# Kernel optimization log

Hardware: AMD Instinct MI355X
Metric: run time of the kernel (lower is better)

Reference implementation:

```python
import jax, jax.numpy as jnp
import numpy as np

# dims: T time steps, B batch, CIN/COUT conv channels, HxW spatial, K kernel
T, B, CIN, COUT, H, Wd, K = 10, 32, 3, 64, 64, 64, 3
DECAY = 0.2      # LIF leak factor
INH = 1.625      # lateral inhibition strength (mode='threshold')


def setup_inputs() -> dict:
    key = jax.random.key(0)
    k1, k2 = jax.random.split(key)
    x = (jax.random.uniform(k1, (T, B, CIN, H, Wd)) < 0.2).astype(jnp.float32)
    W = jax.random.normal(k2, (COUT, CIN, K, K), dtype=jnp.float32)
    # normweight(): zero-mean, unit-std (biased) per output filter
    W = W - W.mean(axis=(1, 2, 3), keepdims=True)
    W = W / W.reshape(COUT, -1).std(axis=1).reshape(COUT, 1, 1, 1)
    return {"x": x, "W": W}


def _conv(x, W):
    # Conv2d stride=1, padding=1, no bias, NCHW/OIHW
    return jax.lax.conv_general_dilated(
        x, W, window_strides=(1, 1), padding=((1, 1), (1, 1)),
        dimension_numbers=("NCHW", "OIHW", "NCHW"))


def reference(x, W):
    def step(mem, x_t):
        i = _conv(x_t, W)                                        # (B,COUT,H,W)
        # ATB: adaptive per-channel threshold = max over batch+spatial
        thr = jnp.max(i, axis=(0, 2, 3), keepdims=True) + 1e-4   # (1,COUT,1,1)
        # ASF: clamp then thresholded sigmoid filter
        cur = jnp.maximum(i, 0.0)
        i_asf = thr * jax.nn.sigmoid((cur - 0.4 * thr) * (8.0 / thr))
        # LIF update with threshold = thr (set by ATB)
        mem = mem * DECAY + i_asf
        s = (mem > thr).astype(mem.dtype)                        # spikes 0/1
        # WTA k=1: keep only the strongest spiking channel per location
        score = mem * s
        winner = jnp.argmax(score, axis=1)                       # (B,H,W)
        oh = jnp.moveaxis(jax.nn.one_hot(winner, COUT, dtype=mem.dtype), -1, 1)
        s = s * oh
        # membrane reset of fired neurons
        mem = mem * (1.0 - s)
        # lateral inhibition: suppress non-winners at spiking locations
        any_sp = jnp.max(s, axis=1, keepdims=True)
        mem = mem - INH * thr * any_sp * (1.0 - s)
        return mem, s

    mem0 = jnp.zeros((B, COUT, H, Wd), jnp.float32)
    _, spikes = jax.lax.scan(step, mem0, x)
    return spikes  # (T,B,COUT,H,W)
```

## Files before the change

kernel.cpp:

```cpp
#include <hip/hip_runtime.h>
#include <math.h>

#define TT 10
#define BB 32
#define CIN 3
#define COUT 64
#define HH 64
#define WW 64
#define HW (HH*WW)
#define DECAY 0.2f
#define INH 1.625f

__device__ __forceinline__ unsigned int enc_f(float f) {
    unsigned int u = __float_as_uint(f);
    return (u & 0x80000000u) ? ~u : (u | 0x80000000u);
}
__device__ __forceinline__ float dec_f(unsigned int u) {
    u = (u & 0x80000000u) ? (u & 0x7FFFFFFFu) : ~u;
    return __uint_as_float(u);
}

__global__ __launch_bounds__(256) void thr_kernel(
    const float* __restrict__ x,
    const float* __restrict__ Wt,
    unsigned int* __restrict__ thr_raw,
    float* __restrict__ out)
{
    __shared__ float sx[CIN][6][68];
    __shared__ float wmax[4][COUT];

    const int tid  = threadIdx.x;
    const int lane = tid & 63;
    const int wave = tid >> 6;
    const int h0   = blockIdx.x * 4;
    const int b    = blockIdx.y;
    const int t    = blockIdx.z;

    float w[27];
    #pragma unroll
    for (int k = 0; k < 27; k++) w[k] = Wt[lane * 27 + k];

    const float* xb = x + ((size_t)t * BB + b) * (CIN * HW);
    for (int l = tid; l < CIN * 6 * 66; l += 256) {
        int ci  = l / 396;
        int r   = (l % 396) / 66;
        int col = l % 66;
        int gh = h0 + r - 1;
        int gw = col - 1;
        float v = 0.f;
        if (gh >= 0 && gh < HH && gw >= 0 && gw < WW)
            v = xb[ci * HW + gh * WW + gw];
        sx[ci][r][col] = v;
    }
    __syncthreads();

    {
        float* ob = out + (((size_t)t * BB + b) * COUT) * HW;
        #pragma unroll
        for (int g = 0; g < 16; g++) {
            int l   = g * 256 + tid;
            int row = l >> 4;
            int q   = l & 15;
            int c   = row >> 2;
            int hr  = row & 3;
            *(float4*)(ob + (size_t)c * HW + (h0 + hr) * WW + q * 4) =
                make_float4(0.f, 0.f, 0.f, 0.f);
        }
    }

    float mx = -INFINITY;

    for (int cc = 0; cc < 16; cc++) {
        float acc0 = 0.f, acc1 = 0.f, acc2 = 0.f, acc3 = 0.f;
        #pragma unroll
        for (int ci = 0; ci < CIN; ci++)
            #pragma unroll
            for (int kh = 0; kh < 3; kh++) {
                const float* rp = &sx[ci][wave + kh][cc * 4];
                float4 q = *(const float4*)rp;
                float2 r2 = *(const float2*)(rp + 4);
                float x0 = q.x, x1 = q.y, x2 = q.z, x3 = q.w;
                float x4 = r2.x, x5 = r2.y;
                const float w0 = w[ci * 9 + kh * 3 + 0];
                const float w1 = w[ci * 9 + kh * 3 + 1];
                const float w2 = w[ci * 9 + kh * 3 + 2];
                acc0 = fmaf(w0, x0, acc0); acc0 = fmaf(w1, x1, acc0); acc0 = fmaf(w2, x2, acc0);
                acc1 = fmaf(w0, x1, acc1); acc1 = fmaf(w1, x2, acc1); acc1 = fmaf(w2, x3, acc1);
                acc2 = fmaf(w0, x2, acc2); acc2 = fmaf(w1, x3, acc2); acc2 = fmaf(w2, x4, acc2);
                acc3 = fmaf(w0, x3, acc3); acc3 = fmaf(w1, x4, acc3); acc3 = fmaf(w2, x5, acc3);
            }
        mx = fmaxf(mx, fmaxf(fmaxf(acc0, acc1), fmaxf(acc2, acc3)));
    }

    wmax[wave][lane] = mx;
    __syncthreads();
    if (wave == 0) {
        float m = fmaxf(fmaxf(wmax[0][lane], wmax[1][lane]),
                        fmaxf(wmax[2][lane], wmax[3][lane]));
        atomicMax(&thr_raw[t * COUT + lane], enc_f(m));
    }
}

__global__ __launch_bounds__(256) void fused_kernel(
    const float* __restrict__ x,
    const float* __restrict__ Wt,
    const unsigned int* __restrict__ thr_raw,
    float* __restrict__ out)
{
    __shared__ float sx[5][CIN][3][36];

    const int tid  = threadIdx.x;
    const int lane = tid & 63;
    const int wave = tid >> 6;
    const int p0   = __builtin_amdgcn_readfirstlane(wave * 8);
    const int b    = blockIdx.x >> 7;
    const int h    = (blockIdx.x >> 1) & 63;
    const int w0   = (blockIdx.x & 1) << 5;

    float w[27];
    #pragma unroll
    for (int k = 0; k < 27; k++) w[k] = Wt[lane * 27 + k];

    const float* xb0 = x + (size_t)b * (CIN * HW);

#define STAGE5(T0) {                                                          \
        for (int l = tid; l < 5 * 306; l += 256) {                            \
            int t   = l / 306;                                                \
            int r0  = l - t * 306;                                            \
            int ci  = r0 / 102;                                               \
            int r1  = r0 - ci * 102;                                          \
            int r   = r1 / 34;                                                \
            int col = r1 - r * 34;                                            \
            int gh = h + r - 1;                                               \
            int gw = w0 + col - 1;                                            \
            float v = 0.f;                                                    \
            if (gh >= 0 && gh < HH && gw >= 0 && gw < WW)                     \
                v = xb0[(size_t)((T0) + t) * ((size_t)BB * CIN * HW)          \
                        + ci * HW + gh * WW + gw];                            \
            sx[t][ci][r][col] = v;                                            \
        }                                                                     \
    }

    STAGE5(0);

    float mem[8];
    #pragma unroll
    for (int j = 0; j < 8; j++) mem[j] = 0.f;

    __syncthreads();

    #pragma unroll 1
    for (int t = 0; t < TT; t++) {
        if (t == 5) {
            __syncthreads();
            STAGE5(5);
            __syncthreads();
        }
        const int slot = (t < 5) ? t : t - 5;

        float thr   = dec_f(thr_raw[t * COUT + lane]) + 1e-4f;
        float sinv  = 8.0f / thr;
        float s04   = 0.4f * thr;
        float sinh_ = INH * thr;

        int fmask = 0;

#define LIF_PX(J, ACC) {                                                    \
        float cur = fmaxf(ACC, 0.f);                                        \
        float z   = (cur - s04) * sinv;                                     \
        float sig = 1.0f / (1.0f + expf(-z));                               \
        float m   = mem[J] * DECAY + thr * sig;                             \
        int   sp  = m > thr;                                                \
        float score = sp ? m : 0.f;                                         \
        unsigned long long blt = __ballot(sp);                              \
        int fr = 0, sp_any = 0;                                             \
        if (blt) {                                  \
            float bs = score;                                               \
            int   bc = lane;                                                \
            _Pragma("unroll")                                               \
            for (int off = 32; off > 0; off >>= 1) {                        \
                float so = __shfl_xor(bs, off, 64);                         \
                int   co = __shfl_xor(bc, off, 64);                         \
                if (so > bs || (so == bs && co < bc)) { bs = so; bc = co; } \
            }                                                               \
            int spw = __shfl(sp, bc, 64);      \
            fr     = (lane == bc) && sp;                                    \
            sp_any = spw;                                                   \
        }                                                                   \
        mem[J] = fr ? 0.f : (m - (sp_any ? sinh_ : 0.f));                   \
        if (fr) fmask |= (1 << (J));                                        \
    }

        #pragma unroll
        for (int ch = 0; ch < 2; ch++) {
            const int c0 = p0 + ch * 4;
            float acc0 = 0.f, acc1 = 0.f, acc2 = 0.f, acc3 = 0.f;
            #pragma unroll
            for (int ci = 0; ci < CIN; ci++)
                #pragma unroll
                for (int kh = 0; kh < 3; kh++) {
                    const float* rp = &sx[slot][ci][kh][c0];
                    float4 q = *(const float4*)rp;
                    float2 r2 = *(const float2*)(rp + 4);
                    float x0 = q.x, x1 = q.y, x2 = q.z, x3 = q.w;
                    float x4 = r2.x, x5 = r2.y;
                    const float w0_ = w[ci * 9 + kh * 3 + 0];
                    const float w1_ = w[ci * 9 + kh * 3 + 1];
                    const float w2_ = w[ci * 9 + kh * 3 + 2];
                    acc0 = fmaf(w0_, x0, acc0); acc0 = fmaf(w1_, x1, acc0); acc0 = fmaf(w2_, x2, acc0);
                    acc1 = fmaf(w0_, x1, acc1); acc1 = fmaf(w1_, x2, acc1); acc1 = fmaf(w2_, x3, acc1);
                    acc2 = fmaf(w0_, x2, acc2); acc2 = fmaf(w1_, x3, acc2); acc2 = fmaf(w2_, x4, acc2);
                    acc3 = fmaf(w0_, x3, acc3); acc3 = fmaf(w1_, x4, acc3); acc3 = fmaf(w2_, x5, acc3);
                }
            LIF_PX(ch * 4 + 0, acc0);
            LIF_PX(ch * 4 + 1, acc1);
            LIF_PX(ch * 4 + 2, acc2);
            LIF_PX(ch * 4 + 3, acc3);
        }
#undef LIF_PX

        if (fmask) {
            float* os = out + (((size_t)t * BB + b) * COUT) * HW + h * WW + w0;
            #pragma unroll
            for (int j = 0; j < 8; j++)
                if (fmask & (1 << j))
                    os[(size_t)lane * HW + p0 + j] = 1.0f;
        }
    }
#undef STAGE5
}

extern "C" void kernel_launch(void* const* d_in, const int* in_sizes, int n_in,
                              void* d_out, int out_size, void* d_ws, size_t ws_size,
                              hipStream_t stream) {
    const float* x = (const float*)d_in[0];
    const float* W = (const float*)d_in[1];
    float* out     = (float*)d_out;

    unsigned int* thr = (unsigned int*)d_ws;
    hipMemsetAsync(thr, 0, TT * COUT * sizeof(unsigned int), stream);

    thr_kernel<<<dim3(HH / 4, BB, TT), 256, 0, stream>>>(x, W, thr, out);
    fused_kernel<<<dim3(BB * HH * 2), 256, 0, stream>>>(x, W, thr, out);
}
```

Before: 527.2 us.

## Widen conv register tiles to 8 pixels and stage all timesteps at once

The threshold kernel now computes 8 output pixels per inner iteration and interleaves the zeroing stores of the output with the convolution loop. The fused kernel stages all 10 timesteps of input into shared memory up front, which removes the mid-loop restage and its two barriers. It also computes all 8 pixel accumulators before running the LIF and winner-take-all updates, which gives more independent work between shuffle reductions. The costs are more registers per thread and about twice the shared memory per block, which may lower occupancy.

```diff
diff --git a/kernel.cpp b/kernel.cpp
--- a/kernel.cpp
+++ b/kernel.cpp
@@ -54,11 +54,13 @@
     }
     __syncthreads();
 
-    {
-        float* ob = out + (((size_t)t * BB + b) * COUT) * HW;
-        #pragma unroll
-        for (int g = 0; g < 16; g++) {
-            int l   = g * 256 + tid;
+    float* ob = out + (((size_t)t * BB + b) * COUT) * HW;
+    float mx = -INFINITY;
+
+    for (int cc = 0; cc < 8; cc++) {
+        #pragma unroll
+        for (int k = 0; k < 2; k++) {
+            int l   = (cc * 2 + k) * 256 + tid;
             int row = l >> 4;
             int q   = l & 15;
             int c   = row >> 2;
@@ -66,30 +68,37 @@
             *(float4*)(ob + (size_t)c * HW + (h0 + hr) * WW + q * 4) =
                 make_float4(0.f, 0.f, 0.f, 0.f);
         }
-    }
-
-    float mx = -INFINITY;
-
-    for (int cc = 0; cc < 16; cc++) {
-        float acc0 = 0.f, acc1 = 0.f, acc2 = 0.f, acc3 = 0.f;
+
+        float acc[8];
+        #pragma unroll
+        for (int j = 0; j < 8; j++) acc[j] = 0.f;
+
         #pragma unroll
         for (int ci = 0; ci < CIN; ci++)
             #pragma unroll
             for (int kh = 0; kh < 3; kh++) {
-                const float* rp = &sx[ci][wave + kh][cc * 4];
-                float4 q = *(const float4*)rp;
-                float2 r2 = *(const float2*)(rp + 4);
-                float x0 = q.x, x1 = q.y, x2 = q.z, x3 = q.w;
-                float x4 = r2.x, x5 = r2.y;
+                const float* rp = &sx[ci][wave + kh][cc * 8];
+                float4 qa = *(const float4*)(rp + 0);
+                float4 qb = *(const float4*)(rp + 4);
+                float2 qc = *(const float2*)(rp + 8);
+                float f0 = qa.x, f1 = qa.y, f2 = qa.z, f3 = qa.w;
+                float f4 = qb.x, f5 = qb.y, f6 = qb.z, f7 = qb.w;
+                float f8 = qc.x, f9 = qc.y;
                 const float w0 = w[ci * 9 + kh * 3 + 0];
                 const float w1 = w[ci * 9 + kh * 3 + 1];
                 const float w2 = w[ci * 9 + kh * 3 + 2];
-                acc0 = fmaf(w0, x0, acc0); acc0 = fmaf(w1, x1, acc0); acc0 = fmaf(w2, x2, acc0);
-                acc1 = fmaf(w0, x1, acc1); acc1 = fmaf(w1, x2, acc1); acc1 = fmaf(w2, x3, acc1);
-                acc2 = fmaf(w0, x2, acc2); acc2 = fmaf(w1, x3, acc2); acc2 = fmaf(w2, x4, acc2);
-                acc3 = fmaf(w0, x3, acc3); acc3 = fmaf(w1, x4, acc3); acc3 = fmaf(w2, x5, acc3);
+                acc[0] = fmaf(w0, f0, acc[0]); acc[0] = fmaf(w1, f1, acc[0]); acc[0] = fmaf(w2, f2, acc[0]);
+                acc[1] = fmaf(w0, f1, acc[1]); acc[1] = fmaf(w1, f2, acc[1]); acc[1] = fmaf(w2, f3, acc[1]);
+                acc[2] = fmaf(w0, f2, acc[2]); acc[2] = fmaf(w1, f3, acc[2]); acc[2] = fmaf(w2, f4, acc[2]);
+                acc[3] = fmaf(w0, f3, acc[3]); acc[3] = fmaf(w1, f4, acc[3]); acc[3] = fmaf(w2, f5, acc[3]);
+                acc[4] = fmaf(w0, f4, acc[4]); acc[4] = fmaf(w1, f5, acc[4]); acc[4] = fmaf(w2, f6, acc[4]);
+                acc[5] = fmaf(w0, f5, acc[5]); acc[5] = fmaf(w1, f6, acc[5]); acc[5] = fmaf(w2, f7, acc[5]);
+                acc[6] = fmaf(w0, f6, acc[6]); acc[6] = fmaf(w1, f7, acc[6]); acc[6] = fmaf(w2, f8, acc[6]);
+                acc[7] = fmaf(w0, f7, acc[7]); acc[7] = fmaf(w1, f8, acc[7]); acc[7] = fmaf(w2, f9, acc[7]);
             }
-        mx = fmaxf(mx, fmaxf(fmaxf(acc0, acc1), fmaxf(acc2, acc3)));
+
+        #pragma unroll
+        for (int j = 0; j < 8; j++) mx = fmaxf(mx, acc[j]);
     }
 
     wmax[wave][lane] = mx;
@@ -107,7 +116,7 @@
     const unsigned int* __restrict__ thr_raw,
     float* __restrict__ out)
 {
-    __shared__ float sx[5][CIN][3][36];
+    __shared__ float sx[TT][CIN][3][36];
 
     const int tid  = threadIdx.x;
     const int lane = tid & 63;
@@ -121,27 +130,24 @@
     #pragma unroll
     for (int k = 0; k < 27; k++) w[k] = Wt[lane * 27 + k];
 
-    const float* xb0 = x + (size_t)b * (CIN * HW);
-
-#define STAGE5(T0) {                                                          \
-        for (int l = tid; l < 5 * 306; l += 256) {                            \
-            int t   = l / 306;                                                \
-            int r0  = l - t * 306;                                            \
-            int ci  = r0 / 102;                                               \
-            int r1  = r0 - ci * 102;                                          \
-            int r   = r1 / 34;                                                \
-            int col = r1 - r * 34;                                            \
-            int gh = h + r - 1;                                               \
-            int gw = w0 + col - 1;                                            \
-            float v = 0.f;                                                    \
-            if (gh >= 0 && gh < HH && gw >= 0 && gw < WW)                     \
-                v = xb0[(size_t)((T0) + t) * ((size_t)BB * CIN * HW)          \
-                        + ci * HW + gh * WW + gw];                            \
-            sx[t][ci][r][col] = v;                                            \
-        }                                                                     \
-    }
-
-    STAGE5(0);
+    {
+        const float* xb0 = x + (size_t)b * (CIN * HW);
+        for (int l = tid; l < TT * 306; l += 256) {
+            int t   = l / 306;
+            int r0  = l - t * 306;
+            int ci  = r0 / 102;
+            int r1  = r0 - ci * 102;
+            int r   = r1 / 34;
+            int col = r1 - r * 34;
+            int gh = h + r - 1;
+            int gw = w0 + col - 1;
+            float v = 0.f;
+            if (gh >= 0 && gh < HH && gw >= 0 && gw < WW)
+                v = xb0[(size_t)t * ((size_t)BB * CIN * HW)
+                        + ci * HW + gh * WW + gw];
+            sx[t][ci][r][col] = v;
+        }
+    }
 
     float mem[8];
     #pragma unroll
@@ -151,22 +157,43 @@
 
     #pragma unroll 1
     for (int t = 0; t < TT; t++) {
-        if (t == 5) {
-            __syncthreads();
-            STAGE5(5);
-            __syncthreads();
-        }
-        const int slot = (t < 5) ? t : t - 5;
-
         float thr   = dec_f(thr_raw[t * COUT + lane]) + 1e-4f;
         float sinv  = 8.0f / thr;
         float s04   = 0.4f * thr;
         float sinh_ = INH * thr;
 
+        float acc[8];
+        #pragma unroll
+        for (int j = 0; j < 8; j++) acc[j] = 0.f;
+
+        #pragma unroll
+        for (int ci = 0; ci < CIN; ci++)
+            #pragma unroll
+            for (int kh = 0; kh < 3; kh++) {
+                const float* rp = &sx[t][ci][kh][p0];
+                float4 qa = *(const float4*)(rp + 0);
+                float4 qb = *(const float4*)(rp + 4);
+                float2 qc = *(const float2*)(rp + 8);
+                float f0 = qa.x, f1 = qa.y, f2 = qa.z, f3 = qa.w;
+                float f4 = qb.x, f5 = qb.y, f6 = qb.z, f7 = qb.w;
+                float f8 = qc.x, f9 = qc.y;
+                const float w0_ = w[ci * 9 + kh * 3 + 0];
+                const float w1_ = w[ci * 9 + kh * 3 + 1];
+                const float w2_ = w[ci * 9 + kh * 3 + 2];
+                acc[0] = fmaf(w0_, f0, acc[0]); acc[0] = fmaf(w1_, f1, acc[0]); acc[0] = fmaf(w2_, f2, acc[0]);
+                acc[1] = fmaf(w0_, f1, acc[1]); acc[1] = fmaf(w1_, f2, acc[1]); acc[1] = fmaf(w2_, f3, acc[1]);
+                acc[2] = fmaf(w0_, f2, acc[2]); acc[2] = fmaf(w1_, f3, acc[2]); acc[2] = fmaf(w2_, f4, acc[2]);
+                acc[3] = fmaf(w0_, f3, acc[3]); acc[3] = fmaf(w1_, f4, acc[3]); acc[3] = fmaf(w2_, f5, acc[3]);
+                acc[4] = fmaf(w0_, f4, acc[4]); acc[4] = fmaf(w1_, f5, acc[4]); acc[4] = fmaf(w2_, f6, acc[4]);
+                acc[5] = fmaf(w0_, f5, acc[5]); acc[5] = fmaf(w1_, f6, acc[5]); acc[5] = fmaf(w2_, f7, acc[5]);
+                acc[6] = fmaf(w0_, f6, acc[6]); acc[6] = fmaf(w1_, f7, acc[6]); acc[6] = fmaf(w2_, f8, acc[6]);
+                acc[7] = fmaf(w0_, f7, acc[7]); acc[7] = fmaf(w1_, f8, acc[7]); acc[7] = fmaf(w2_, f9, acc[7]);
+            }
+
         int fmask = 0;
 
-#define LIF_PX(J, ACC) {                                                    \
-        float cur = fmaxf(ACC, 0.f);                                        \
+#define LIF_PX(J) {                                                         \
+        float cur = fmaxf(acc[J], 0.f);                                     \
         float z   = (cur - s04) * sinv;                                     \
         float sig = 1.0f / (1.0f + expf(-z));                               \
         float m   = mem[J] * DECAY + thr * sig;                             \
@@ -191,32 +218,8 @@
         if (fr) fmask |= (1 << (J));                                        \
     }
 
-        #pragma unroll
-        for (int ch = 0; ch < 2; ch++) {
-            const int c0 = p0 + ch * 4;
-            float acc0 = 0.f, acc1 = 0.f, acc2 = 0.f, acc3 = 0.f;
-            #pragma unroll
-            for (int ci = 0; ci < CIN; ci++)
-                #pragma unroll
-                for (int kh = 0; kh < 3; kh++) {
-                    const float* rp = &sx[slot][ci][kh][c0];
-                    float4 q = *(const float4*)rp;
-                    float2 r2 = *(const float2*)(rp + 4);
-                    float x0 = q.x, x1 = q.y, x2 = q.z, x3 = q.w;
-                    float x4 = r2.x, x5 = r2.y;
-                    const float w0_ = w[ci * 9 + kh * 3 + 0];
-                    const float w1_ = w[ci * 9 + kh * 3 + 1];
-                    const float w2_ = w[ci * 9 + kh * 3 + 2];
-                    acc0 = fmaf(w0_, x0, acc0); acc0 = fmaf(w1_, x1, acc0); acc0 = fmaf(w2_, x2, acc0);
-                    acc1 = fmaf(w0_, x1, acc1); acc1 = fmaf(w1_, x2, acc1); acc1 = fmaf(w2_, x3, acc1);
-                    acc2 = fmaf(w0_, x2, acc2); acc2 = fmaf(w1_, x3, acc2); acc2 = fmaf(w2_, x4, acc2);
-                    acc3 = fmaf(w0_, x3, acc3); acc3 = fmaf(w1_, x4, acc3); acc3 = fmaf(w2_, x5, acc3);
-                }
-            LIF_PX(ch * 4 + 0, acc0);
-            LIF_PX(ch * 4 + 1, acc1);
-            LIF_PX(ch * 4 + 2, acc2);
-            LIF_PX(ch * 4 + 3, acc3);
-        }
+        LIF_PX(0); LIF_PX(1); LIF_PX(2); LIF_PX(3);
+        LIF_PX(4); LIF_PX(5); LIF_PX(6); LIF_PX(7);
 #undef LIF_PX
 
         if (fmask) {
@@ -227,7 +230,6 @@
                     os[(size_t)lane * HW + p0 + j] = 1.0f;
         }
     }
-#undef STAGE5
 }
 
 extern "C" void kernel_launch(void* const* d_in, const int* in_sizes, int n_in,
```

Measured after the change: 523.4 us. No clear change (-0.7%).
